# Optimization experiments

Measured on AMD Instinct MI355X. Metric: run time of the kernel, lower is better.

The kernel has to match this reference:

```python
import jax, jax.numpy as jnp
import numpy as np

T = 0.1  # temperature (init kwarg)
NEG_INF = -1e9


def setup_inputs() -> dict:
    key = jax.random.key(0)
    k1, k2 = jax.random.split(key)
    B, N, D = 4096, 2, 128
    feats = jax.random.normal(k1, (B, N, D), dtype=jnp.float32)
    labels = jax.random.randint(k2, (B,), 0, 512, dtype=jnp.int64)
    return {"feats": feats, "labels": labels}


def reference(feats, labels):
    B, N, D = feats.shape
    M = B * N
    f = feats.reshape(M, D)
    # F.normalize(dim=1): L2 normalize rows with eps clamp
    norm = jnp.maximum(jnp.linalg.norm(f, axis=1, keepdims=True), 1e-12)
    f = f / norm
    # labels.unsqueeze(1).repeat(1, N).view(-1)
    lab = jnp.repeat(labels, N)  # [M]
    mask = (lab[:, None] == lab[None, :]).astype(f.dtype)  # [M, M]
    logits = (f @ f.T) / T  # [M, M]
    logits_mask = 1.0 - jnp.eye(M, dtype=f.dtype)
    mask = mask * logits_mask  # drop self-pairs
    logits = logits * logits_mask + NEG_INF * (1.0 - logits_mask)
    log_prob = logits - jax.nn.logsumexp(logits, axis=1, keepdims=True)
    mean_pos = (mask * log_prob).sum(axis=1) / mask.sum(axis=1)
    return -mean_pos.mean()
```

## Files before the change

kernel.cpp:

```cpp
#include <hip/hip_runtime.h>
#include <math.h>

#define DD 128
#define NSPLIT 24
#define NBINS 512
#define SHIFT 10.0f
#define L2E_T 14.4269504089f

typedef _Float16 f16x8 __attribute__((ext_vector_type(8)));
typedef _Float16 f16x2 __attribute__((ext_vector_type(2)));
typedef float f32x4 __attribute__((ext_vector_type(4)));

__device__ __forceinline__ float ex2(float x) {
#if __has_builtin(__builtin_amdgcn_exp2f)
    return __builtin_amdgcn_exp2f(x);
#else
    return exp2f(x);
#endif
}

__global__ __launch_bounds__(256)
void zero_kernel(int* __restrict__ hist, float* __restrict__ out)
{
    hist[threadIdx.x] = 0;
    hist[256 + threadIdx.x] = 0;
    if (threadIdx.x == 0) out[0] = 0.f;
}

__global__ __launch_bounds__(256)
void norm_kernel(const float* __restrict__ f, const int* __restrict__ labels,
                 _Float16* __restrict__ fh, int* __restrict__ labm,
                 int* __restrict__ hist, int M, int nrep)
{
    int gw = (blockIdx.x * 256 + threadIdx.x) >> 6;
    int lane = threadIdx.x & 63;
    if (gw >= M) return;
    float2 v = *reinterpret_cast<const float2*>(&f[(size_t)gw * DD + lane * 2]);
    float ss = v.x * v.x + v.y * v.y;
    #pragma unroll
    for (int m = 1; m < 64; m <<= 1) ss += __shfl_xor(ss, m);
    float inv = 1.0f / fmaxf(sqrtf(ss), 1e-12f);
    f16x2 h; h[0] = (_Float16)(v.x * inv); h[1] = (_Float16)(v.y * inv);
    *reinterpret_cast<f16x2*>(&fh[(size_t)gw * DD + lane * 2]) = h;
    if (lane == 0) {
        int lb = labels[gw / nrep];
        labm[gw] = lb;
        if ((gw % nrep) == 0) atomicAdd(&hist[lb], nrep);
    }
}

__global__ __launch_bounds__(256, 3)
void supcon_main(const _Float16* __restrict__ fh, const int* __restrict__ labm,
                 float* __restrict__ Epart, float* __restrict__ Ppart,
                 int M, int nsub_total)
{
    const int lane = threadIdx.x & 63;
    const int w = threadIdx.x >> 6;
    const int ibase = blockIdx.x * 256 + w * 64;
    const int rowsel = lane & 15;
    const int grp = lane >> 4;
    const int ksel = grp * 8;

    f16x8 bfr[4][4];
    #pragma unroll
    for (int t = 0; t < 4; ++t)
        #pragma unroll
        for (int kk = 0; kk < 4; ++kk)
            bfr[t][kk] = *reinterpret_cast<const f16x8*>(
                &fh[(size_t)(ibase + t * 16 + rowsel) * DD + kk * 32 + ksel]);

    int li[4];
    #pragma unroll
    for (int t = 0; t < 4; ++t) li[t] = labm[ibase + t * 16 + rowsel];

    float esum[4] = {0.f, 0.f, 0.f, 0.f};
    float psum[4] = {0.f, 0.f, 0.f, 0.f};

    const int base = nsub_total / NSPLIT, rem = nsub_total % NSPLIT;
    const int by = blockIdx.y;
    const int s0 = by * base + (by < rem ? by : rem);
    const int send = s0 + base + (by < rem ? 1 : 0);

    const _Float16* aptr = fh + (size_t)rowsel * DD + ksel;
    const int* lptr = labm + grp * 4;

#define LOADT(A, L, s) { \
    _Pragma("unroll") for (int kk = 0; kk < 4; ++kk) \
        A[kk] = *reinterpret_cast<const f16x8*>(aptr + (size_t)(s) * 16 * DD + kk * 32); \
    L = *reinterpret_cast<const int4*>(lptr + (s) * 16); }

#define MFMA16(A, c0, c1, c2, c3) { \
    _Pragma("unroll") for (int kk = 0; kk < 4; ++kk) { \
        c0 = __builtin_amdgcn_mfma_f32_16x16x32_f16(A[kk], bfr[0][kk], c0, 0, 0, 0); \
        c1 = __builtin_amdgcn_mfma_f32_16x16x32_f16(A[kk], bfr[1][kk], c1, 0, 0, 0); \
        c2 = __builtin_amdgcn_mfma_f32_16x16x32_f16(A[kk], bfr[2][kk], c2, 0, 0, 0); \
        c3 = __builtin_amdgcn_mfma_f32_16x16x32_f16(A[kk], bfr[3][kk], c3, 0, 0, 0); } }

#define EPI1(t, cc, L) { \
    esum[t] += (ex2(__builtin_fmaf(cc[0], L2E_T, -L2E_T)) \
              + ex2(__builtin_fmaf(cc[1], L2E_T, -L2E_T))) \
             + (ex2(__builtin_fmaf(cc[2], L2E_T, -L2E_T)) \
              + ex2(__builtin_fmaf(cc[3], L2E_T, -L2E_T))); \
    float p0 = (L.x == li[t]) ? cc[0] : 0.f; \
    float p1 = (L.y == li[t]) ? cc[1] : 0.f; \
    float p2 = (L.z == li[t]) ? cc[2] : 0.f; \
    float p3 = (L.w == li[t]) ? cc[3] : 0.f; \
    psum[t] += (p0 + p1) + (p2 + p3); }

#define EPI4(c0, c1, c2, c3, L) { \
    EPI1(0, c0, L); EPI1(1, c1, L); EPI1(2, c2, L); EPI1(3, c3, L); }

    f16x8 af0[4], af1[4];
    int4 lj0, lj1;
    LOADT(af0, lj0, s0);

    int s = s0;
    for (; s + 1 < send; s += 2) {
        {
            f32x4 c0 = {0,0,0,0}, c1 = {0,0,0,0}, c2 = {0,0,0,0}, c3 = {0,0,0,0};
            MFMA16(af0, c0, c1, c2, c3);
            LOADT(af1, lj1, s + 1);
            EPI4(c0, c1, c2, c3, lj0);
        }
        {
            f32x4 c0 = {0,0,0,0}, c1 = {0,0,0,0}, c2 = {0,0,0,0}, c3 = {0,0,0,0};
            MFMA16(af1, c0, c1, c2, c3);
            if (s + 2 < send) LOADT(af0, lj0, s + 2);
            EPI4(c0, c1, c2, c3, lj1);
        }
    }
    if (s < send) {
        f32x4 c0 = {0,0,0,0}, c1 = {0,0,0,0}, c2 = {0,0,0,0}, c3 = {0,0,0,0};
        MFMA16(af0, c0, c1, c2, c3);
        EPI4(c0, c1, c2, c3, lj0);
    }
#undef LOADT
#undef MFMA16
#undef EPI1
#undef EPI4

    #pragma unroll
    for (int t = 0; t < 4; ++t) {
        float e = esum[t], p = psum[t];
        e += __shfl_xor(e, 16); e += __shfl_xor(e, 32);
        p += __shfl_xor(p, 16); p += __shfl_xor(p, 32);
        if (lane < 16) {
            size_t o = (size_t)by * M + ibase + t * 16 + lane;
            Epart[o] = e;
            Ppart[o] = p;
        }
    }
}

__global__ __launch_bounds__(256)
void final_fused(const _Float16* __restrict__ fh, const float* __restrict__ Epart,
                 const float* __restrict__ Ppart, const int* __restrict__ labm,
                 const int* __restrict__ hist, float* __restrict__ out, int M)
{
    __shared__ float red[4];
    const int i = blockIdx.x * 256 + threadIdx.x;
    float aii = 0.f;
    const f16x8* fr = reinterpret_cast<const f16x8*>(&fh[(size_t)i * DD]);
    #pragma unroll
    for (int k = 0; k < 16; ++k) {
        f16x8 hv = fr[k];
        #pragma unroll
        for (int e = 0; e < 8; ++e) {
            float x = (float)hv[e];
            aii = __builtin_fmaf(x, x, aii);
        }
    }
    float E = 0.f, P = 0.f;
    #pragma unroll
    for (int k = 0; k < NSPLIT; ++k) {
        E += Epart[(size_t)k * M + i];
        P += Ppart[(size_t)k * M + i];
    }
    int lb = labm[i];
    float cnt = (float)(hist[lb] - 1);
    E -= ex2(__builtin_fmaf(aii, L2E_T, -L2E_T));
    float term = (SHIFT + logf(E)) - SHIFT * (P - aii) / cnt;

    #pragma unroll
    for (int m = 1; m < 64; m <<= 1) term += __shfl_xor(term, m);
    int lane = threadIdx.x & 63, wv = threadIdx.x >> 6;
    if (lane == 0) red[wv] = term;
    __syncthreads();
    if (threadIdx.x == 0)
        atomicAdd(out, (red[0] + red[1] + red[2] + red[3]) / (float)M);
}

extern "C" void kernel_launch(void* const* d_in, const int* in_sizes, int n_in,
                              void* d_out, int out_size, void* d_ws, size_t ws_size,
                              hipStream_t stream)
{
    const float* feats = (const float*)d_in[0];
    const int* labels = (const int*)d_in[1];
    const int Bn = in_sizes[1];
    const int M = in_sizes[0] / DD;
    const int nrep = M / Bn;

    char* ws = (char*)d_ws;
    _Float16* fh = (_Float16*)ws;
    size_t off = (size_t)M * DD * sizeof(_Float16);
    int* labm = (int*)(ws + off); off += (size_t)M * sizeof(int);
    int* hist = (int*)(ws + off); off += (size_t)NBINS * sizeof(int);
    off = (off + 255) & ~(size_t)255;
    float* Epart = (float*)(ws + off); off += (size_t)NSPLIT * M * sizeof(float);
    float* Ppart = (float*)(ws + off); off += (size_t)NSPLIT * M * sizeof(float);

    zero_kernel<<<1, 256, 0, stream>>>(hist, (float*)d_out);

    norm_kernel<<<M / 4, 256, 0, stream>>>(feats, labels, fh, labm, hist, M, nrep);

    const int nsub_total = M / 16;
    dim3 grid(M / 256, NSPLIT);
    supcon_main<<<grid, 256, 0, stream>>>(fh, labm, Epart, Ppart, M, nsub_total);

    final_fused<<<M / 256, 256, 0, stream>>>(fh, Epart, Ppart, labm, hist,
                                             (float*)d_out, M);
}
```

Baseline: 58.56 us.

## Stage shared j-tiles in LDS with swizzled double buffer across waves

```diff
diff --git a/kernel.cpp b/kernel.cpp
--- a/kernel.cpp
+++ b/kernel.cpp
@@ -54,8 +54,12 @@
                  float* __restrict__ Epart, float* __restrict__ Ppart,
                  int M, int nsub_total)
 {
-    const int lane = threadIdx.x & 63;
-    const int w = threadIdx.x >> 6;
+    __shared__ float4 jbuf[2][1024];
+    __shared__ int    jlab[2][64];
+
+    const int tid = threadIdx.x;
+    const int lane = tid & 63;
+    const int w = tid >> 6;
     const int ibase = blockIdx.x * 256 + w * 64;
     const int rowsel = lane & 15;
     const int grp = lane >> 4;
@@ -80,14 +84,33 @@
     const int by = blockIdx.y;
     const int s0 = by * base + (by < rem ? by : rem);
     const int send = s0 + base + (by < rem ? 1 : 0);
-
-    const _Float16* aptr = fh + (size_t)rowsel * DD + ksel;
-    const int* lptr = labm + grp * 4;
-
-#define LOADT(A, L, s) { \
-    _Pragma("unroll") for (int kk = 0; kk < 4; ++kk) \
-        A[kk] = *reinterpret_cast<const f16x8*>(aptr + (size_t)(s) * 16 * DD + kk * 32); \
-    L = *reinterpret_cast<const int4*>(lptr + (s) * 16); }
+    const int nsub = send - s0;
+    const int nb = (nsub + 3) >> 2;
+    const int rowmax = nsub_total * 16 - 1;
+
+    int srow[4], sc4[4];
+    #pragma unroll
+    for (int p = 0; p < 4; ++p) {
+        int g = p * 256 + tid;
+        srow[p] = g >> 4;
+        sc4[p] = g & 15;
+    }
+
+    float4 R[4];
+    int labR = 0;
+
+#define STAGE_LOAD(tt) { \
+    const int rb = (s0 + (tt) * 4) * 16; \
+    _Pragma("unroll") for (int p = 0; p < 4; ++p) { \
+        int rr = rb + srow[p]; if (rr > rowmax) rr = rowmax; \
+        R[p] = *reinterpret_cast<const float4*>(&fh[(size_t)rr * DD + sc4[p] * 8]); } \
+    if (tid < 64) { int rr = rb + tid; if (rr > rowmax) rr = rowmax; labR = labm[rr]; } }
+
+#define STAGE_WRITE(bb) { \
+    _Pragma("unroll") for (int p = 0; p < 4; ++p) { \
+        int slot = srow[p] * 16 + (sc4[p] ^ (srow[p] & 7)); \
+        jbuf[bb][slot] = R[p]; } \
+    if (tid < 64) jlab[bb][tid] = labR; }
 
 #define MFMA16(A, c0, c1, c2, c3) { \
     _Pragma("unroll") for (int kk = 0; kk < 4; ++kk) { \
@@ -110,34 +133,38 @@
 #define EPI4(c0, c1, c2, c3, L) { \
     EPI1(0, c0, L); EPI1(1, c1, L); EPI1(2, c2, L); EPI1(3, c3, L); }
 
-    f16x8 af0[4], af1[4];
-    int4 lj0, lj1;
-    LOADT(af0, lj0, s0);
-
-    int s = s0;
-    for (; s + 1 < send; s += 2) {
-        {
-            f32x4 c0 = {0,0,0,0}, c1 = {0,0,0,0}, c2 = {0,0,0,0}, c3 = {0,0,0,0};
-            MFMA16(af0, c0, c1, c2, c3);
-            LOADT(af1, lj1, s + 1);
-            EPI4(c0, c1, c2, c3, lj0);
+#define COMPUTE(bb, tt) { \
+    const int nv = ((tt) == nb - 1) ? (nsub - (nb - 1) * 4) : 4; \
+    _Pragma("unroll") for (int k = 0; k < 4; ++k) { \
+        if (k < nv) { \
+            f16x8 af[4]; \
+            const int row = k * 16 + rowsel; \
+            _Pragma("unroll") for (int kk = 0; kk < 4; ++kk) { \
+                int slot = row * 16 + ((grp + kk * 4) ^ (row & 7)); \
+                af[kk] = *reinterpret_cast<const f16x8*>(&jbuf[bb][slot]); } \
+            const int4 lj = *reinterpret_cast<const int4*>(&jlab[bb][k * 16 + grp * 4]); \
+            f32x4 c0 = {0,0,0,0}, c1 = {0,0,0,0}, c2 = {0,0,0,0}, c3 = {0,0,0,0}; \
+            MFMA16(af, c0, c1, c2, c3); \
+            EPI4(c0, c1, c2, c3, lj); } } }
+
+    STAGE_LOAD(0);
+    STAGE_WRITE(0);
+    __syncthreads();
+    for (int t = 0; t < nb; ++t) {
+        if (t + 1 < nb) STAGE_LOAD(t + 1);
+        COMPUTE(t & 1, t);
+        __syncthreads();
+        if (t + 1 < nb) {
+            STAGE_WRITE((t + 1) & 1);
+            __syncthreads();
         }
-        {
-            f32x4 c0 = {0,0,0,0}, c1 = {0,0,0,0}, c2 = {0,0,0,0}, c3 = {0,0,0,0};
-            MFMA16(af1, c0, c1, c2, c3);
-            if (s + 2 < send) LOADT(af0, lj0, s + 2);
-            EPI4(c0, c1, c2, c3, lj1);
-        }
-    }
-    if (s < send) {
-        f32x4 c0 = {0,0,0,0}, c1 = {0,0,0,0}, c2 = {0,0,0,0}, c3 = {0,0,0,0};
-        MFMA16(af0, c0, c1, c2, c3);
-        EPI4(c0, c1, c2, c3, lj0);
-    }
-#undef LOADT
+    }
+#undef STAGE_LOAD
+#undef STAGE_WRITE
 #undef MFMA16
 #undef EPI1
 #undef EPI4
+#undef COMPUTE
 
     #pragma unroll
     for (int t = 0; t < 4; ++t) {
```

Result: slower. 112.4 us (+92.0%).
